# Kernel tuning notes

Measured on AMD Instinct MI355X. Metric: run time of the kernel, lower is better.

## Reference

```python
import jax, jax.numpy as jnp
import numpy as np

D_MODEL = 1024
H = 16
D_K = D_MODEL // H
B = 4
S = 2048


def setup_inputs() -> dict:
    key = jax.random.key(0)
    ks = jax.random.split(key, 7)
    q = jax.random.normal(ks[0], (B, S, D_MODEL), dtype=jnp.float32)
    k = jax.random.normal(ks[1], (B, S, D_MODEL), dtype=jnp.float32)
    v = jax.random.normal(ks[2], (B, S, D_MODEL), dtype=jnp.float32)
    # nn.Linear weights have shape (out_features, in_features); y = x @ W.T
    scale = 1.0 / np.sqrt(D_MODEL)
    w_q = jax.random.normal(ks[3], (D_MODEL, D_MODEL), dtype=jnp.float32) * scale
    w_k = jax.random.normal(ks[4], (D_MODEL, D_MODEL), dtype=jnp.float32) * scale
    w_v = jax.random.normal(ks[5], (D_MODEL, D_MODEL), dtype=jnp.float32) * scale
    w_o = jax.random.normal(ks[6], (D_MODEL, D_MODEL), dtype=jnp.float32) * scale
    mask = jnp.ones((1, 1, S, S), dtype=bool)  # broadcasts over [B,H,S,S]
    return {"q": q, "k": k, "v": v, "w_q": w_q, "w_k": w_k, "w_v": w_v,
            "w_o": w_o, "mask": mask}


def reference(q, k, v, w_q, w_k, w_v, w_o, mask):
    # projections (nn.Linear, no bias): x @ W.T
    query = jnp.einsum('bsd,ed->bse', q, w_q)
    key_p = jnp.einsum('bsd,ed->bse', k, w_k)
    value = jnp.einsum('bsd,ed->bse', v, w_v)
    # split heads: [B,S,D] -> [B,H,S,d_k]
    query = query.reshape(B, S, H, D_K).transpose(0, 2, 1, 3)
    key_p = key_p.reshape(B, S, H, D_K).transpose(0, 2, 1, 3)
    value = value.reshape(B, S, H, D_K).transpose(0, 2, 1, 3)
    # scaled dot-product attention (explicit softmax, as in source)
    scores = jnp.einsum('bhqd,bhkd->bhqk', query, key_p) / jnp.sqrt(
        jnp.asarray(D_K, dtype=query.dtype))
    scores = jnp.where(mask, scores, jnp.asarray(-1e9, dtype=scores.dtype))
    weights = jax.nn.softmax(scores, axis=-1)
    ctx = jnp.einsum('bhqk,bhkd->bhqd', weights, value)
    # merge heads and output projection
    ctx = ctx.transpose(0, 2, 1, 3).reshape(B, S, D_MODEL)
    return jnp.einsum('bsd,ed->bse', ctx, w_o)
```

## Files before the change

kernel.cpp:

```cpp
#include <hip/hip_runtime.h>
#include <hip/hip_bf16.h>
#include <stdint.h>
#include <math.h>

#define DM 1024
#define SS 2048
#define HH 16

typedef unsigned short u16;
typedef __attribute__((ext_vector_type(8))) short short8;
typedef __attribute__((ext_vector_type(4))) float f32x4;
typedef __attribute__((ext_vector_type(4))) unsigned short u16x4;

#define C_SCALE 0.18033688011112042f

__device__ __forceinline__ u16 f2bf(float f) {
    union { float f; uint32_t u; } v; v.f = f;
    uint32_t r = v.u + 0x7FFFu + ((v.u >> 16) & 1u);
    return (u16)(r >> 16);
}

__device__ __forceinline__ void async_cp16(const void* g, void* l) {
    __builtin_amdgcn_global_load_lds(
        reinterpret_cast<const __attribute__((address_space(1))) unsigned int*>(
            reinterpret_cast<uintptr_t>(g)),
        reinterpret_cast<__attribute__((address_space(3))) unsigned int*>(
            reinterpret_cast<uintptr_t>(l)),
        16, 0, 0);
}

__device__ __forceinline__ short8 pack8(const float4 a, const float4 b) {
    union { short8 s; struct { __hip_bfloat162 p0, p1, p2, p3; } p; } u;
    u.p.p0 = __float22bfloat162_rn(make_float2(a.x, a.y));
    u.p.p1 = __float22bfloat162_rn(make_float2(a.z, a.w));
    u.p.p2 = __float22bfloat162_rn(make_float2(b.x, b.y));
    u.p.p3 = __float22bfloat162_rn(make_float2(b.z, b.w));
    return u.s;
}

__global__ __launch_bounds__(256) void cast_w4(const float* __restrict__ w0,
                                               const float* __restrict__ w1,
                                               const float* __restrict__ w2,
                                               const float* __restrict__ w3,
                                               u16* __restrict__ o0,
                                               u16* __restrict__ o1,
                                               u16* __restrict__ o2,
                                               u16* __restrict__ o3)
{
    const uint32_t which = blockIdx.x >> 10;
    const uint32_t i = (blockIdx.x & 1023u) * 256u + threadIdx.x;
    const float* in = which == 0 ? w0 : which == 1 ? w1 : which == 2 ? w2 : w3;
    u16* out = which == 0 ? o0 : which == 1 ? o1 : which == 2 ? o2 : o3;
    float4 v = ((const float4*)in)[i];
    u16x4 p = { f2bf(v.x), f2bf(v.y), f2bf(v.z), f2bf(v.w) };
    ((u16x4*)out)[i] = p;
}

__global__ __launch_bounds__(256) void gemm_castA3(const float* __restrict__ Aq,
                                                   const float* __restrict__ Ak,
                                                   const float* __restrict__ Av,
                                                   const u16* __restrict__ Bq,
                                                   const u16* __restrict__ Bk,
                                                   const u16* __restrict__ Bv,
                                                   u16* __restrict__ Cq,
                                                   u16* __restrict__ Ck,
                                                   u16* __restrict__ Cv)
{
    __shared__ char sm[49152];
    const uint32_t t = threadIdx.x;
    const uint32_t l = t & 63u, w = t >> 6;
    const uint32_t sw = (blockIdx.x & 7u) * 192u + (blockIdx.x >> 3);
    const uint32_t which = sw >> 9;
    const uint32_t inner = sw & 511u;
    const uint32_t bm = inner >> 3, bn = inner & 7u;
    const uint32_t wr = w >> 1, wc = w & 1u;

    const float* A = which == 0 ? Aq : which == 1 ? Ak : Av;
    const u16*   B = which == 0 ? Bq : which == 1 ? Bk : Bv;

    const uint32_t q15 = l & 15u, G = l >> 4, xq = q15 & 7u;
    const uint32_t vA0  = wr * 16384u + q15 * 256u + ((2u * G ^ xq) << 4);
    const uint32_t vA0x = vA0 ^ 16u;
    const uint32_t vbg0 = q15 * 128u + ((G ^ (xq & 3u)) << 4) + ((xq >> 2) << 6);
    const uint32_t vB0 = 32768u + wc * 8192u + vbg0, vB1 = vB0 ^ 64u;

    uint32_t LA[8];
    const float* aP[8];
    #pragma unroll
    for (uint32_t i = 0; i < 8; ++i) {
        const uint32_t j = i * 256u + t, row = j >> 4, ch = j & 15u;
        const uint32_t c8 = ch ^ (row & 7u);
        aP[i] = A + (size_t)(bm * 128u + row) * DM + c8 * 4u;
        LA[i] = j * 16u;
    }
    uint32_t LB[4];
    const u16* bP[4];
    #pragma unroll
    for (uint32_t i = 0; i < 4; ++i) {
        LB[i] = (i * 256u + t) * 16u;
        const uint32_t r = LB[i] >> 7;
        const uint32_t c8 = ((LB[i] >> 4) & 7u) ^ (r & 7u);
        bP[i] = B + (size_t)(bn * 128u + r) * DM + c8 * 8u;
    }

    f32x4 acc[4][4] = {};

    for (uint32_t k0 = 0; k0 < 1024; k0 += 64) {
        __syncthreads();
        #pragma unroll
        for (uint32_t i = 0; i < 8; ++i) async_cp16(aP[i] + k0, sm + LA[i]);
        #pragma unroll
        for (uint32_t i = 0; i < 4; ++i) async_cp16(bP[i] + k0, sm + 32768 + LB[i]);
        __syncthreads();

        #pragma unroll
        for (uint32_t kk = 0; kk < 2; ++kk) {
            const uint32_t ao = kk * 128u;
            const uint32_t vb = kk ? vB1 : vB0;
            short8 a[4], bfr[4];
            #pragma unroll
            for (uint32_t m = 0; m < 4; ++m) {
                float4 lo = *(const float4*)(sm + vA0  + ao + m * 4096u);
                float4 hi = *(const float4*)(sm + vA0x + ao + m * 4096u);
                a[m] = pack8(lo, hi);
            }
            #pragma unroll
            for (uint32_t n = 0; n < 4; ++n)
                bfr[n] = *(const short8*)(sm + vb + n * 2048u);
            #pragma unroll
            for (uint32_t m = 0; m < 4; ++m)
                #pragma unroll
                for (uint32_t n = 0; n < 4; ++n)
                    acc[m][n] = __builtin_amdgcn_mfma_f32_16x16x32_bf16(
                        a[m], bfr[n], acc[m][n], 0, 0, 0);
        }
    }

    u16* Cb = which == 0 ? Cq : which == 1 ? Ck : Cv;
    const float sc = which == 0 ? C_SCALE : 1.0f;
    #pragma unroll
    for (uint32_t m = 0; m < 4; ++m) {
        #pragma unroll
        for (uint32_t n = 0; n < 4; ++n) {
            const uint32_t rmb = bm * 128u + wr * 64u + m * 16u + G * 4u;
            const uint32_t cn  = bn * 128u + wc * 64u + n * 16u + q15;
            if (which != 2) {
                #pragma unroll
                for (uint32_t g = 0; g < 4; ++g)
                    Cb[(size_t)(rmb + g) * DM + cn] = f2bf(acc[m][n][g] * sc);
            } else {
                const uint32_t b_ = rmb >> 11, s0 = rmb & 2047u;
                u16x4 pk;
                #pragma unroll
                for (uint32_t g = 0; g < 4; ++g) pk[g] = f2bf(acc[m][n][g]);
                *(u16x4*)(Cb + (size_t)(b_ * 1024u + cn) * 2048u + s0) = pk;
            }
        }
    }
}

__global__ __launch_bounds__(256) void gemm_out(const u16* __restrict__ A,
                                                const u16* __restrict__ B,
                                                float* __restrict__ C)
{
    __shared__ char sm[65536];
    const uint32_t t = threadIdx.x;
    const uint32_t l = t & 63u, w = t >> 6;
    uint32_t id = blockIdx.x;
    id = (id & 7u) * 64u + (id >> 3);
    const uint32_t bm = id >> 3, bn = id & 7u;
    const uint32_t wr = w >> 1, wc = w & 1u;

    const uint32_t q15 = l & 15u, G = l >> 4, xq = q15 & 7u;
    const uint32_t vbg0 = q15 * 128u + ((G ^ (xq & 3u)) << 4) + ((xq >> 2) << 6);
    const uint32_t vA0 = wr * 8192u + vbg0,          vA1 = vA0 ^ 64u;
    const uint32_t vB0 = 16384u + wc * 8192u + vbg0, vB1 = vB0 ^ 64u;

    uint32_t La[4];
    const u16* aP[4];
    const u16* bP[4];
    #pragma unroll
    for (uint32_t i = 0; i < 4; ++i) {
        La[i] = (i * 256u + t) * 16u;
        const uint32_t r = La[i] >> 7;
        const uint32_t c8 = ((La[i] >> 4) & 7u) ^ (r & 7u);
        aP[i] = A + (size_t)(bm * 128u + r) * DM + c8 * 8u;
        bP[i] = B + (size_t)(bn * 128u + r) * DM + c8 * 8u;
    }

    f32x4 acc[4][4] = {};

    #pragma unroll
    for (uint32_t i = 0; i < 4; ++i) async_cp16(aP[i], sm + La[i]);
    #pragma unroll
    for (uint32_t i = 0; i < 4; ++i) async_cp16(bP[i], sm + 16384 + La[i]);

#define GEMM_STEP(CURB, STGB, STG, MODE)                                       \
    {                                                                          \
        if ((MODE) == 0) {                                                     \
            _Pragma("unroll")                                                  \
            for (uint32_t i = 0; i < 4; ++i)                                   \
                async_cp16(aP[i] + (STG), sm + (STGB) + La[i]);                \
            _Pragma("unroll")                                                  \
            for (uint32_t i = 0; i < 4; ++i)                                   \
                async_cp16(bP[i] + (STG), sm + (STGB) + 16384u + La[i]);       \
            asm volatile("s_waitcnt vmcnt(8)" ::: "memory");                   \
        } else {                                                               \
            asm volatile("s_waitcnt vmcnt(0)" ::: "memory");                   \
        }                                                                      \
        __builtin_amdgcn_s_barrier();                                          \
        __builtin_amdgcn_sched_barrier(0);                                     \
        _Pragma("unroll")                                                      \
        for (uint32_t kk = 0; kk < 2; ++kk) {                                  \
            const uint32_t va = (CURB) + (kk ? vA1 : vA0);                     \
            const uint32_t vb = (CURB) + (kk ? vB1 : vB0);                     \
            short8 a[4], b[4];                                                 \
            _Pragma("unroll")                                                  \
            for (uint32_t m = 0; m < 4; ++m)                                   \
                a[m] = *(const short8*)(sm + va + m * 2048u);                  \
            _Pragma("unroll")                                                  \
            for (uint32_t n = 0; n < 4; ++n)                                   \
                b[n] = *(const short8*)(sm + vb + n * 2048u);                  \
            __builtin_amdgcn_s_setprio(1);                                     \
            _Pragma("unroll")                                                  \
            for (uint32_t m = 0; m < 4; ++m)                                   \
                _Pragma("unroll")                                              \
                for (uint32_t n = 0; n < 4; ++n)                               \
                    acc[m][n] = __builtin_amdgcn_mfma_f32_16x16x32_bf16(       \
                        a[m], b[n], acc[m][n], 0, 0, 0);                       \
            __builtin_amdgcn_s_setprio(0);                                     \
        }                                                                      \
        asm volatile("s_waitcnt lgkmcnt(0)" ::: "memory");                     \
        __builtin_amdgcn_s_barrier();                                          \
        __builtin_amdgcn_sched_barrier(0);                                     \
    }

    for (uint32_t it = 0; it < 7; ++it) {
        GEMM_STEP(0u,     32768u, it * 128u + 64u,  0)
        GEMM_STEP(32768u, 0u,     it * 128u + 128u, 0)
    }
    GEMM_STEP(0u,     32768u, 960u, 0)
    GEMM_STEP(32768u, 0u,     0u,   1)

#undef GEMM_STEP

    #pragma unroll
    for (uint32_t m = 0; m < 4; ++m) {
        #pragma unroll
        for (uint32_t n = 0; n < 4; ++n) {
            const uint32_t rmb = bm * 128u + wr * 64u + m * 16u + G * 4u;
            const uint32_t cn  = bn * 128u + wc * 64u + n * 16u + q15;
            #pragma unroll
            for (uint32_t g = 0; g < 4; ++g)
                C[(size_t)(rmb + g) * DM + cn] = acc[m][n][g];
        }
    }
}

__global__ __launch_bounds__(512) void attn_mfma(const u16* __restrict__ Q,
                                                 const u16* __restrict__ K,
                                                 const u16* __restrict__ Vt,
                                                 u16* __restrict__ ctx)
{
    __shared__ char sm[69632];
    const uint32_t t = threadIdx.x, l = t & 63u, w = t >> 6;
    uint32_t id = blockIdx.x;
    id = (id & 7u) * 64u + (id >> 3);
    const uint32_t qt = id & 7u, h = (id >> 3) & 15u, b = id >> 7;

    const uint32_t q15 = l & 15u, G = l >> 4, xq = q15 & 7u;

    const uint32_t vb0 = q15 * 128u + ((G ^ (xq & 3u)) << 4) + ((xq >> 2) << 6);
    const uint32_t vb1 = vb0 ^ 64u;
    const uint32_t vbPw = w * 4608u + q15 * 144u + G * 8u;
    const uint32_t vbPr = w * 4608u + q15 * 144u + G * 16u;

    short8 qf[2][2];
    #pragma unroll
    for (uint32_t qb = 0; qb < 2; ++qb) {
        const size_t qrow = (size_t)(b * 2048u + qt * 256u + w * 32u + qb * 16u + q15);
        const uint32_t col = h * 64u + (G << 3);
        qf[qb][0] = *(const short8*)(Q + qrow * DM + col);
        qf[qb][1] = *(const short8*)(Q + qrow * DM + col + 32u);
    }

    short8 ones;
    #pragma unroll
    for (int i = 0; i < 8; ++i) ones[i] = (short)0x3F80;
    const f32x4 ZV = {0.f, 0.f, 0.f, 0.f};

    f32x4 o[2][4] = {};
    f32x4 osum[2] = {};

    const uint32_t Ls = t * 16u;
    const u16* kcur;
    const u16* vcur;
    {
        const size_t kbase = (size_t)b * 2048u * DM + h * 64u;
        const size_t vbase = (size_t)((b * 16u + h) * 64u) * 2048u;
        const uint32_t r = Ls >> 7;
        const uint32_t c8 = ((Ls >> 4) & 7u) ^ (r & 7u);
        const u16* k0p = K  + kbase + (size_t)r * DM    + c8 * 8u;
        const u16* v0p = Vt + vbase + (size_t)r * 2048u + c8 * 8u;
        async_cp16(k0p, sm + Ls);
        async_cp16(v0p, sm + 8192 + Ls);
        kcur = k0p + (size_t)64u * DM;
        vcur = v0p + 64u;
    }

#define ATTN_STEP(BCc, BNc, STAGE)                                             \
    {                                                                          \
        if (STAGE) {                                                           \
            async_cp16(kcur, sm + (BNc) + Ls);                                 \
            async_cp16(vcur, sm + (BNc) + 8192u + Ls);                         \
            kcur += (size_t)64u * DM;                                          \
            vcur += 64u;                                                       \
            asm volatile("s_waitcnt vmcnt(2)" ::: "memory");                   \
        } else {                                                               \
            asm volatile("s_waitcnt vmcnt(0)" ::: "memory");                   \
        }                                                                      \
        __builtin_amdgcn_s_barrier();                                          \
        __builtin_amdgcn_sched_barrier(0);                                     \
        f32x4 s[2][4];                                                         \
        __builtin_amdgcn_s_setprio(1);                                         \
        _Pragma("unroll")                                                      \
        for (uint32_t mf = 0; mf < 4; ++mf) {                                  \
            short8 kf0 = *(const short8*)(sm + (BCc) + vb0 + mf * 2048u);      \
            short8 kf1 = *(const short8*)(sm + (BCc) + vb1 + mf * 2048u);      \
            _Pragma("unroll")                                                  \
            for (uint32_t qb = 0; qb < 2; ++qb) {                              \
                s[qb][mf] = __builtin_amdgcn_mfma_f32_16x16x32_bf16(           \
                    kf1, qf[qb][1],                                            \
                    __builtin_amdgcn_mfma_f32_16x16x32_bf16(                   \
                        kf0, qf[qb][0], ZV, 0, 0, 0),                          \
                    0, 0, 0);                                                  \
            }                                                                  \
        }                                                                      \
        __builtin_amdgcn_s_setprio(0);                                         \
        _Pragma("unroll")                                                      \
        for (uint32_t qb = 0; qb < 2; ++qb) {                                  \
            _Pragma("unroll")                                                  \
            for (uint32_t mf = 0; mf < 4; ++mf) {                              \
                float p0 = __builtin_amdgcn_exp2f(s[qb][mf][0]);               \
                float p1 = __builtin_amdgcn_exp2f(s[qb][mf][1]);               \
                float p2 = __builtin_amdgcn_exp2f(s[qb][mf][2]);               \
                float p3 = __builtin_amdgcn_exp2f(s[qb][mf][3]);               \
                union { u16x4 v; struct { __hip_bfloat162 lo, hi; } b; } pk;   \
                pk.b.lo = __float22bfloat162_rn(make_float2(p0, p1));          \
                pk.b.hi = __float22bfloat162_rn(make_float2(p2, p3));          \
                *(u16x4*)(sm + 32768u + vbPw + qb * 2304u + mf * 32u) = pk.v;  \
            }                                                                  \
        }                                                                      \
        _Pragma("unroll")                                                      \
        for (uint32_t kk = 0; kk < 2; ++kk) {                                  \
            const uint32_t vv = (kk ? vb1 : vb0) + 8192u;                      \
            short8 vf[4];                                                      \
            _Pragma("unroll")                                                  \
            for (uint32_t d = 0; d < 4; ++d)                                   \
                vf[d] = *(const short8*)(sm + (BCc) + vv + d * 2048u);         \
            __builtin_amdgcn_s_setprio(1);                                     \
            _Pragma("unroll")                                                  \
            for (uint32_t qb = 0; qb < 2; ++qb) {                              \
                short8 pf = *(const short8*)(sm + 32768u + vbPr +              \
                                             qb * 2304u + kk * 64u);           \
                _Pragma("unroll")                                              \
                for (uint32_t d = 0; d < 4; ++d)                               \
                    o[qb][d] = __builtin_amdgcn_mfma_f32_16x16x32_bf16(        \
                        pf, vf[d], o[qb][d], 0, 0, 0);                         \
                osum[qb] = __builtin_amdgcn_mfma_f32_16x16x32_bf16(            \
                    pf, ones, osum[qb], 0, 0, 0);                              \
            }                                                                  \
            __builtin_amdgcn_s_setprio(0);                                     \
        }                                                                      \
        asm volatile("s_waitcnt lgkmcnt(0)" ::: "memory");                     \
        __builtin_amdgcn_s_barrier();                                          \
        __builtin_amdgcn_sched_barrier(0);                                     \
    }

    for (uint32_t it = 0; it < 15; ++it) {
        ATTN_STEP(0u, 16384u, true)
        ATTN_STEP(16384u, 0u, true)
    }
    ATTN_STEP(0u, 16384u, true)
    ATTN_STEP(16384u, 0u, false)

#undef ATTN_STEP

    #pragma unroll
    for (uint32_t qb = 0; qb < 2; ++qb) {
        float inv[4];
        #pragma unroll
        for (int g = 0; g < 4; ++g) inv[g] = 1.0f / osum[qb][g];
        #pragma unroll
        for (uint32_t d = 0; d < 4; ++d)
            #pragma unroll
            for (int g = 0; g < 4; ++g) {
                const uint32_t srow = qt * 256u + w * 32u + qb * 16u + G * 4u + (uint32_t)g;
                const uint32_t col  = h * 64u + d * 16u + q15;
                ctx[(size_t)(b * 2048u + srow) * DM + col] = f2bf(o[qb][d][g] * inv[g]);
            }
    }
}

extern "C" void kernel_launch(void* const* d_in, const int* in_sizes, int n_in,
                              void* d_out, int out_size, void* d_ws, size_t ws_size,
                              hipStream_t stream)
{
    const float* q  = (const float*)d_in[0];
    const float* k  = (const float*)d_in[1];
    const float* v  = (const float*)d_in[2];
    const float* wq = (const float*)d_in[3];
    const float* wk = (const float*)d_in[4];
    const float* wv = (const float*)d_in[5];
    const float* wo = (const float*)d_in[6];

    const size_t SZ = (size_t)4 * 2048 * 1024;
    const size_t WZ = (size_t)1024 * 1024;
    u16* ctx = (u16*)d_ws;
    u16* Qp  = ctx + SZ;
    u16* Kp  = Qp  + SZ;
    u16* Vtp = Kp  + SZ;
    u16* wqb = Vtp + SZ;
    u16* wkb = wqb + WZ;
    u16* wvb = wkb + WZ;
    u16* wob = wvb + WZ;

    cast_w4<<<4096, 256, 0, stream>>>(wq, wk, wv, wo, wqb, wkb, wvb, wob);

    gemm_castA3<<<1536, 256, 0, stream>>>(q, k, v, wqb, wkb, wvb, Qp, Kp, Vtp);

    attn_mfma<<<512, 512, 0, stream>>>(Qp, Kp, Vtp, ctx);

    gemm_out<<<512, 256, 0, stream>>>(ctx, wob, (float*)d_out);
}
```

Baseline: 178.2 us.

## Double-buffer projection GEMM LDS tiles with K=32 steps and async prefetch

The QKV projection GEMM previously loaded a 64-wide K tile into a single LDS buffer, with barriers before and after each load. It now uses two 24 KB buffers with 32-wide K steps, issuing the next tile's async global-to-LDS copies before computing on the current one. A partial vmcnt wait lets the loads overlap the MFMA work, and s_setprio raises priority around the MFMA block. The cost is twice as many barrier rounds per K, a new B-tile swizzle layout, and reliance on hand-counted vmcnt values for correctness.

```diff
diff --git a/kernel.cpp b/kernel.cpp
--- a/kernel.cpp
+++ b/kernel.cpp
@@ -79,62 +79,84 @@
     const u16*   B = which == 0 ? Bq : which == 1 ? Bk : Bv;
 
     const uint32_t q15 = l & 15u, G = l >> 4, xq = q15 & 7u;
-    const uint32_t vA0  = wr * 16384u + q15 * 256u + ((2u * G ^ xq) << 4);
+    const uint32_t vA0  = wr * 8192u + q15 * 128u + (((2u * G) ^ xq) << 4);
     const uint32_t vA0x = vA0 ^ 16u;
-    const uint32_t vbg0 = q15 * 128u + ((G ^ (xq & 3u)) << 4) + ((xq >> 2) << 6);
-    const uint32_t vB0 = 32768u + wc * 8192u + vbg0, vB1 = vB0 ^ 64u;
-
-    uint32_t LA[8];
-    const float* aP[8];
-    #pragma unroll
-    for (uint32_t i = 0; i < 8; ++i) {
-        const uint32_t j = i * 256u + t, row = j >> 4, ch = j & 15u;
-        const uint32_t c8 = ch ^ (row & 7u);
-        aP[i] = A + (size_t)(bm * 128u + row) * DM + c8 * 4u;
+    const uint32_t r2 = q15 >> 1;
+    const uint32_t vB0 = 16384u + wc * 4096u + r2 * 128u +
+                         ((((((q15 & 1u) << 2) | G)) ^ r2) << 4);
+
+    uint32_t LA[4];
+    const float* aP[4];
+    #pragma unroll
+    for (uint32_t i = 0; i < 4; ++i) {
+        const uint32_t j = i * 256u + t, row = j >> 3, c = j & 7u;
+        const uint32_t c2 = c ^ (row & 7u);
+        aP[i] = A + (size_t)(bm * 128u + row) * DM + c2 * 4u;
         LA[i] = j * 16u;
     }
-    uint32_t LB[4];
-    const u16* bP[4];
-    #pragma unroll
-    for (uint32_t i = 0; i < 4; ++i) {
-        LB[i] = (i * 256u + t) * 16u;
-        const uint32_t r = LB[i] >> 7;
-        const uint32_t c8 = ((LB[i] >> 4) & 7u) ^ (r & 7u);
-        bP[i] = B + (size_t)(bn * 128u + r) * DM + c8 * 8u;
+    uint32_t LB[2];
+    const u16* bP[2];
+    #pragma unroll
+    for (uint32_t i = 0; i < 2; ++i) {
+        const uint32_t j = i * 256u + t, lr = j >> 3, c = j & 7u;
+        const uint32_t c2 = c ^ (lr & 7u);
+        bP[i] = B + (size_t)(bn * 128u + 2u * lr + (c2 >> 2)) * DM + (c2 & 3u) * 8u;
+        LB[i] = 16384u + j * 16u;
     }
 
     f32x4 acc[4][4] = {};
 
-    for (uint32_t k0 = 0; k0 < 1024; k0 += 64) {
-        __syncthreads();
-        #pragma unroll
-        for (uint32_t i = 0; i < 8; ++i) async_cp16(aP[i] + k0, sm + LA[i]);
-        #pragma unroll
-        for (uint32_t i = 0; i < 4; ++i) async_cp16(bP[i] + k0, sm + 32768 + LB[i]);
-        __syncthreads();
-
-        #pragma unroll
-        for (uint32_t kk = 0; kk < 2; ++kk) {
-            const uint32_t ao = kk * 128u;
-            const uint32_t vb = kk ? vB1 : vB0;
-            short8 a[4], bfr[4];
-            #pragma unroll
-            for (uint32_t m = 0; m < 4; ++m) {
-                float4 lo = *(const float4*)(sm + vA0  + ao + m * 4096u);
-                float4 hi = *(const float4*)(sm + vA0x + ao + m * 4096u);
-                a[m] = pack8(lo, hi);
-            }
-            #pragma unroll
-            for (uint32_t n = 0; n < 4; ++n)
-                bfr[n] = *(const short8*)(sm + vb + n * 2048u);
-            #pragma unroll
-            for (uint32_t m = 0; m < 4; ++m)
-                #pragma unroll
-                for (uint32_t n = 0; n < 4; ++n)
-                    acc[m][n] = __builtin_amdgcn_mfma_f32_16x16x32_bf16(
-                        a[m], bfr[n], acc[m][n], 0, 0, 0);
-        }
-    }
+    #pragma unroll
+    for (uint32_t i = 0; i < 4; ++i) async_cp16(aP[i], sm + LA[i]);
+    #pragma unroll
+    for (uint32_t i = 0; i < 2; ++i) async_cp16(bP[i], sm + LB[i]);
+
+#define CA3_STEP(CURB, STGB, KOFF, MODE)                                       \
+    {                                                                          \
+        if ((MODE) == 0) {                                                     \
+            _Pragma("unroll")                                                  \
+            for (uint32_t i = 0; i < 4; ++i)                                   \
+                async_cp16(aP[i] + (KOFF), sm + (STGB) + LA[i]);               \
+            _Pragma("unroll")                                                  \
+            for (uint32_t i = 0; i < 2; ++i)                                   \
+                async_cp16(bP[i] + (KOFF), sm + (STGB) + LB[i]);               \
+            asm volatile("s_waitcnt vmcnt(6)" ::: "memory");                   \
+        } else {                                                               \
+            asm volatile("s_waitcnt vmcnt(0)" ::: "memory");                   \
+        }                                                                      \
+        __builtin_amdgcn_s_barrier();                                          \
+        __builtin_amdgcn_sched_barrier(0);                                     \
+        short8 a[4], bfr[4];                                                   \
+        _Pragma("unroll")                                                      \
+        for (uint32_t m = 0; m < 4; ++m) {                                     \
+            float4 lo = *(const float4*)(sm + (CURB) + vA0  + m * 2048u);      \
+            float4 hi = *(const float4*)(sm + (CURB) + vA0x + m * 2048u);      \
+            a[m] = pack8(lo, hi);                                              \
+        }                                                                      \
+        _Pragma("unroll")                                                      \
+        for (uint32_t n = 0; n < 4; ++n)                                       \
+            bfr[n] = *(const short8*)(sm + (CURB) + vB0 + n * 1024u);          \
+        __builtin_amdgcn_s_setprio(1);                                         \
+        _Pragma("unroll")                                                      \
+        for (uint32_t m = 0; m < 4; ++m)                                       \
+            _Pragma("unroll")                                                  \
+            for (uint32_t n = 0; n < 4; ++n)                                   \
+                acc[m][n] = __builtin_amdgcn_mfma_f32_16x16x32_bf16(           \
+                    a[m], bfr[n], acc[m][n], 0, 0, 0);                         \
+        __builtin_amdgcn_s_setprio(0);                                         \
+        asm volatile("s_waitcnt lgkmcnt(0)" ::: "memory");                     \
+        __builtin_amdgcn_s_barrier();                                          \
+        __builtin_amdgcn_sched_barrier(0);                                     \
+    }
+
+    for (uint32_t it = 0; it < 15; ++it) {
+        CA3_STEP(0u,     24576u, (2u * it + 1u) * 32u, 0)
+        CA3_STEP(24576u, 0u,     (2u * it + 2u) * 32u, 0)
+    }
+    CA3_STEP(0u,     24576u, 992u, 0)
+    CA3_STEP(24576u, 0u,     0u,   1)
+
+#undef CA3_STEP
 
     u16* Cb = which == 0 ? Cq : which == 1 ? Ck : Cv;
     const float sc = which == 0 ? C_SCALE : 1.0f;
```

After: 192.4 us. +8.0%, slower.
